# Kernel tuning notes

Measured on AMD Instinct MI355X. Metric: run time of the kernel, lower is better.

## Reference

```python
import math
import jax, jax.numpy as jnp
import numpy as np

N_HEADS = 16
N_KV_HEADS = 4
HEAD_DIM = 128
D_MODEL = 2048
THETA = 10000.0
SCALE_BASE = 512


def _rope_cos_sin(seq_len, head_dim, theta):
    half = head_dim // 2
    inv_freq = 1.0 / theta ** (jnp.arange(half, dtype=jnp.float32) / half)
    pos = jnp.arange(seq_len, dtype=jnp.float32)
    freqs = jnp.outer(pos, inv_freq)  # (S, half)
    freqs = jnp.concatenate([freqs, freqs], axis=-1)  # (S, D)
    return jnp.cos(freqs), jnp.sin(freqs)


def _rotate_half(x):
    half = x.shape[-1] // 2
    return jnp.concatenate([-x[..., half:], x[..., :half]], axis=-1)


def _xpos_scale(seq_len, head_dim, scale_base):
    pos = jnp.arange(seq_len, dtype=jnp.float32)
    scale = (pos + scale_base / 2.0) / scale_base  # (S,)
    half = head_dim // 2
    s = jnp.broadcast_to(scale[:, None], (seq_len, half))
    # interleave: even idx -> scale, odd idx -> 1/scale
    return jnp.stack([s, 1.0 / s], axis=-1).reshape(seq_len, head_dim)


def setup_inputs() -> dict:
    key = jax.random.key(0)
    ks = jax.random.split(key, 5)
    std = 1.0 / math.sqrt(D_MODEL)
    x = jax.random.normal(ks[0], (2, 2048, D_MODEL), dtype=jnp.float32)
    Wq = jax.random.normal(ks[1], (D_MODEL, N_HEADS * HEAD_DIM), dtype=jnp.float32) * std
    Wk = jax.random.normal(ks[2], (D_MODEL, N_KV_HEADS * HEAD_DIM), dtype=jnp.float32) * std
    Wv = jax.random.normal(ks[3], (D_MODEL, N_KV_HEADS * HEAD_DIM), dtype=jnp.float32) * std
    Wo = jax.random.normal(ks[4], (N_HEADS * HEAD_DIM, D_MODEL), dtype=jnp.float32) * std
    return {"x": x, "Wq": Wq, "Wk": Wk, "Wv": Wv, "Wo": Wo}


def reference(x, Wq, Wk, Wv, Wo):
    B, S, _ = x.shape
    kv_groups = N_HEADS // N_KV_HEADS

    q = (x @ Wq).reshape(B, S, N_HEADS, HEAD_DIM).transpose(0, 2, 1, 3)     # (B,H,S,D)
    k = (x @ Wk).reshape(B, S, N_KV_HEADS, HEAD_DIM).transpose(0, 2, 1, 3)  # (B,Hk,S,D)
    v = (x @ Wv).reshape(B, S, N_KV_HEADS, HEAD_DIM).transpose(0, 2, 1, 3)

    cos, sin = _rope_cos_sin(S, HEAD_DIM, THETA)
    cos = cos[None, None]
    sin = sin[None, None]
    q = q * cos + _rotate_half(q) * sin
    k = k * cos + _rotate_half(k) * sin
    xscale = _xpos_scale(S, HEAD_DIM, SCALE_BASE)[None, None]
    q = q * xscale
    k = k * (1.0 / xscale)

    # GQA: expand kv heads to full head count
    k = jnp.repeat(k, kv_groups, axis=1)  # (B,H,S,D)
    v = jnp.repeat(v, kv_groups, axis=1)

    scale = math.sqrt(HEAD_DIM)
    scores = jnp.einsum('bhqd,bhkd->bhqk', q, k) / scale
    causal = jnp.tril(jnp.ones((S, S), dtype=bool))
    scores = jnp.where(causal[None, None], scores, -jnp.inf)
    attn = jax.nn.softmax(scores, axis=-1)
    out = jnp.einsum('bhqk,bhkd->bhqd', attn, v)
    out = out.transpose(0, 2, 1, 3).reshape(B, S, N_HEADS * HEAD_DIM)
    return out @ Wo
```

## Files before the change

### kernel.cpp

```cpp
#include <hip/hip_runtime.h>
#include <math.h>

#define BDIM 2
#define SLEN 2048
#define NH 16
#define NKV 4
#define HD 128

typedef __attribute__((ext_vector_type(8))) short short8v;
typedef __attribute__((ext_vector_type(4))) short short4v;
typedef __attribute__((ext_vector_type(8))) __bf16 bf16x8;
typedef __attribute__((ext_vector_type(4))) float f32x4;
typedef __attribute__((ext_vector_type(16))) float f32x16;
typedef __attribute__((ext_vector_type(4))) unsigned int u32x4;

__device__ inline unsigned short f2bf(float x) {
  unsigned int u = __builtin_bit_cast(unsigned int, x);
  unsigned int r = (u + 0x7fffu + ((u >> 16) & 1u)) >> 16;
  return (unsigned short)r;
}
__device__ inline float bf2f(unsigned short b) {
  unsigned int u = ((unsigned int)b) << 16;
  return __builtin_bit_cast(float, u);
}
__device__ inline unsigned int pk2(float a, float b) {
  unsigned short ua = __builtin_bit_cast(unsigned short, (__bf16)a);
  unsigned short ub = __builtin_bit_cast(unsigned short, (__bf16)b);
  return (unsigned int)ua | ((unsigned int)ub << 16);
}

template <bool BF16_OUT, bool SPLIT>
__global__ __launch_bounds__(256) void gemm_mfma_bt(
    const unsigned short* __restrict__ A, const unsigned short* __restrict__ Bt,
    void* __restrict__ C0, void* __restrict__ C1,
    int M, int N, int K, int Nsplit, int S0, int S1) {
  __shared__ __align__(16) unsigned short As[128 * 64];
  __shared__ __align__(16) unsigned short Bs[128 * 64];
  const int t    = threadIdx.x;
  const int lane = t & 63;
  const int w    = t >> 6;
  const int lg   = lane >> 4, l15 = lane & 15;
  const int wr   = w >> 1,    wc  = w & 1;
  const int bm = blockIdx.y * 128, bn = blockIdx.x * 128;

  const int srow = w * 32 + (lane >> 3);
  const int scol = (lane & 7) * 8;
  const unsigned short* gA = &A[(size_t)(bm + srow) * K + scol];
  const unsigned short* gB = &Bt[(size_t)(bn + srow) * K + scol];

  f32x4 acc[4][4];
#pragma unroll
  for (int m = 0; m < 4; ++m)
#pragma unroll
    for (int n = 0; n < 4; ++n) acc[m][n] = (f32x4){0.f, 0.f, 0.f, 0.f};

  for (int k0 = 0; k0 < K; k0 += 64) {
    __syncthreads();
#pragma unroll
    for (int i = 0; i < 4; ++i) {
      __builtin_amdgcn_global_load_lds(
          (const __attribute__((address_space(1))) unsigned int*)(gA + (size_t)i * 8 * K + k0),
          (__attribute__((address_space(3))) unsigned int*)&As[(w * 32 + i * 8) * 64],
          16, 0, 0);
      __builtin_amdgcn_global_load_lds(
          (const __attribute__((address_space(1))) unsigned int*)(gB + (size_t)i * 8 * K + k0),
          (__attribute__((address_space(3))) unsigned int*)&Bs[(w * 32 + i * 8) * 64],
          16, 0, 0);
    }
    __syncthreads();
#pragma unroll
    for (int kk = 0; kk < 2; ++kk) {
      bf16x8 a[4], b[4];
#pragma unroll
      for (int m = 0; m < 4; ++m)
        a[m] = __builtin_bit_cast(bf16x8, *reinterpret_cast<const short8v*>(
            &As[(wr * 64 + m * 16 + l15) * 64 + kk * 32 + lg * 8]));
#pragma unroll
      for (int n = 0; n < 4; ++n)
        b[n] = __builtin_bit_cast(bf16x8, *reinterpret_cast<const short8v*>(
            &Bs[(wc * 64 + n * 16 + l15) * 64 + kk * 32 + lg * 8]));
#pragma unroll
      for (int m = 0; m < 4; ++m)
#pragma unroll
        for (int n = 0; n < 4; ++n)
          acc[m][n] = __builtin_amdgcn_mfma_f32_16x16x32_bf16(a[m], b[n], acc[m][n], 0, 0, 0);
    }
  }

  void* dst;
  int col0, stride;
  if (!SPLIT || bn < Nsplit) {
    dst = C0; col0 = bn; stride = S0;
  } else {
    dst = C1; col0 = bn - Nsplit; stride = S1;
  }
#pragma unroll
  for (int m = 0; m < 4; ++m) {
#pragma unroll
    for (int j = 0; j < 4; ++j) {
      const size_t row = (size_t)(bm + wr * 64 + m * 16 + lg * 4 + j);
#pragma unroll
      for (int n = 0; n < 4; ++n) {
        const int col = col0 + wc * 64 + n * 16 + l15;
        if (BF16_OUT)
          ((unsigned short*)dst)[row * stride + col] = f2bf(acc[m][n][j]);
        else
          ((float*)dst)[row * stride + col] = acc[m][n][j];
      }
    }
  }
}

__global__ __launch_bounds__(256) void transpose_cast(
    const float* __restrict__ W, unsigned short* __restrict__ Wt, int K, int N) {
  __shared__ float tile[32][33];
  const int tx = threadIdx.x & 31, ty = threadIdx.x >> 5;
  const int n0 = blockIdx.x * 32, k0 = blockIdx.y * 32;
#pragma unroll
  for (int i = 0; i < 4; ++i)
    tile[ty + i * 8][tx] = W[(size_t)(k0 + ty + i * 8) * N + n0 + tx];
  __syncthreads();
#pragma unroll
  for (int i = 0; i < 4; ++i)
    Wt[(size_t)(n0 + ty + i * 8) * K + k0 + tx] = f2bf(tile[tx][ty + i * 8]);
}

__global__ __launch_bounds__(256) void cast_f32_bf16(
    const float* __restrict__ in, unsigned short* __restrict__ out) {
  const int i = (blockIdx.x * 256 + threadIdx.x) * 8;
  float4 a = *reinterpret_cast<const float4*>(&in[i]);
  float4 b = *reinterpret_cast<const float4*>(&in[i + 4]);
  short8v s;
  s[0] = f2bf(a.x); s[1] = f2bf(a.y); s[2] = f2bf(a.z); s[3] = f2bf(a.w);
  s[4] = f2bf(b.x); s[5] = f2bf(b.y); s[6] = f2bf(b.z); s[7] = f2bf(b.w);
  *reinterpret_cast<short8v*>(&out[i]) = s;
}

__global__ __launch_bounds__(256) void rope_xpos_ip(
    unsigned short* __restrict__ buf, int row_stride, int nh_shift, int invert,
    float extra_scale) {
  const int idx = blockIdx.x * 256 + threadIdx.x;
  const int dp  = idx & 63;
  const int tmp = idx >> 6;
  const int h   = tmp & ((1 << nh_shift) - 1);
  const int row = tmp >> nh_shift;
  const int s   = row & (SLEN - 1);

  const float inv_freq = expf(-(float)dp * (9.210340371976184f / 64.0f));
  const float ang = (float)s * inv_freq;
  float sn, cs;
  sincosf(ang, &sn, &cs);

  unsigned short* p = buf + (size_t)row * row_stride + h * HD;
  const float x0 = bf2f(p[dp]);
  const float x1 = bf2f(p[dp + 64]);
  float y0 = x0 * cs - x1 * sn;
  float y1 = x1 * cs + x0 * sn;

  const float scl = ((float)s + 256.0f) / 512.0f;
  float se_even = invert ? (1.0f / scl) : scl;
  float se_odd  = invert ? scl : (1.0f / scl);
  float se = ((dp & 1) ? se_odd : se_even) * extra_scale;

  p[dp]      = f2bf(y0 * se);
  p[dp + 64] = f2bf(y1 * se);
}

__global__ __launch_bounds__(512) void flash_attn_v9(
    const unsigned short* __restrict__ qb, const unsigned short* __restrict__ kvb,
    unsigned short* __restrict__ o) {
  const int bid = blockIdx.x;
  const int u   = bid & 7;
  const int bh  = bid >> 3;
  const int h   = bh & (NH - 1);
  const int b   = bh >> 4;
  const int kvh = h >> 2;

  __shared__ __align__(16) unsigned char smem[65536];

  const int t    = threadIdx.x;
  const int lane = t & 63;
  const int w    = t >> 6;
  const int par  = w >> 2;
  const int wq   = w & 3;
  const int hi   = lane >> 5;
  const int l31  = lane & 31;

  const size_t bS = (size_t)b * SLEN;

  const int vr2 = t & 31;
  const int vg  = t >> 5;
  int krow[2], kgrp[2];
#pragma unroll
  for (int i = 0; i < 2; ++i) {
    const int slot = w * 2048 + i * 1024 + lane * 16;
    krow[i] = slot >> 8;
    kgrp[i] = (slot >> 4) & 15;
  }

#define K_STAGE(kt, bufk)                                                      \
  { _Pragma("unroll") for (int i = 0; i < 2; ++i) {                            \
      const unsigned short* ksrc = &kvb[(bS + (size_t)(kt) * 64 + krow[i]) * 1024 \
          + kvh * 128 + ((kgrp[i] ^ (krow[i] & 15)) << 3)];                    \
      __builtin_amdgcn_global_load_lds(                                        \
          (const __attribute__((address_space(1))) unsigned int*)ksrc,         \
          (__attribute__((address_space(3))) unsigned int*)                    \
              (smem + (bufk) * 16384 + w * 2048 + i * 1024),                   \
          16, 0, 0); } }

#define V_LOAD(kt, r0, r1)                                                     \
  { const size_t vb_ = (bS + (size_t)(kt) * 64) * 1024 + kvh * 128 + 512;      \
    r0 = *reinterpret_cast<const short8v*>(                                    \
        &kvb[vb_ + (size_t)(2 * vr2) * 1024 + vg * 8]);                        \
    r1 = *reinterpret_cast<const short8v*>(                                    \
        &kvb[vb_ + (size_t)(2 * vr2 + 1) * 1024 + vg * 8]); }

#define V_WRITE(bufk, r0, r1)                                                  \
  { unsigned int* Vw_ = (unsigned int*)(smem + 32768 + (bufk) * 16384);        \
    _Pragma("unroll") for (int j = 0; j < 8; ++j) {                            \
      const int d = vg * 8 + j;                                                \
      Vw_[d * 32 + (vr2 ^ ((d & 7) << 2))] =                                   \
          (unsigned int)(unsigned short)r0[j] |                                \
          ((unsigned int)(unsigned short)r1[j] << 16); } }

  for (int half = 0; half < 2; ++half) {
    const int qt2 = half ? (15 - u) : u;

    bf16x8 qf[8];
    {
      const size_t qrow = (bS + qt2 * 128 + wq * 32 + l31) * 2048 + (size_t)h * HD;
#pragma unroll
      for (int c = 0; c < 8; ++c)
        qf[c] = __builtin_bit_cast(bf16x8,
            *reinterpret_cast<const short8v*>(&qb[qrow + c * 16 + hi * 8]));
    }

    f32x16 Od[4];
#pragma unroll
    for (int ds = 0; ds < 4; ++ds)
#pragma unroll
      for (int r = 0; r < 16; ++r) Od[ds][r] = 0.f;
    float m_run = -1e30f, l_run = 0.f;

    short8v va0, va1, vb0, vb1;

    K_STAGE(0, 0)
    K_STAGE(1, 1)
    V_LOAD(0, va0, va1)
    V_LOAD(1, vb0, vb1)
    V_WRITE(0, va0, va1)
    V_WRITE(1, vb0, vb1)
    __syncthreads();

    for (int e = 0; e <= qt2; ++e) {
      const int kt = 2 * e + par;
      const bool more = (e < qt2);
      if (more) {
        V_LOAD(2 * e + 2, va0, va1)
        V_LOAD(2 * e + 3, vb0, vb1)
      }
      const unsigned short* Kb = (const unsigned short*)(smem + par * 16384);
      const unsigned int*   Vw = (const unsigned int*)(smem + 32768 + par * 16384);

      f32x16 Sa, Sb;
#pragma unroll
      for (int r = 0; r < 16; ++r) { Sa[r] = 0.f; Sb[r] = 0.f; }
      __builtin_amdgcn_s_setprio(1);
#pragma unroll
      for (int c = 0; c < 8; ++c) {
        const int ra = l31, rb = 32 + l31;
        bf16x8 ka = __builtin_bit_cast(bf16x8, *reinterpret_cast<const short8v*>(
            &Kb[ra * 128 + (((2 * c + hi) ^ (ra & 15)) << 3)]));
        bf16x8 kb2 = __builtin_bit_cast(bf16x8, *reinterpret_cast<const short8v*>(
            &Kb[rb * 128 + (((2 * c + hi) ^ (rb & 15)) << 3)]));
        Sa = __builtin_amdgcn_mfma_f32_32x32x16_bf16(ka, qf[c], Sa, 0, 0, 0);
        Sb = __builtin_amdgcn_mfma_f32_32x32x16_bf16(kb2, qf[c], Sb, 0, 0, 0);
      }
      __builtin_amdgcn_s_setprio(0);

      if (kt >= 2 * qt2) {
        const int thresh = qt2 * 128 + wq * 32 + l31 - kt * 64;
#pragma unroll
        for (int r = 0; r < 16; ++r) {
          const int kla = (r & 3) + 8 * (r >> 2) + 4 * hi;
          if (kla > thresh) Sa[r] = -INFINITY;
          if (kla + 32 > thresh) Sb[r] = -INFINITY;
        }
      }

      float pmax = Sa[0];
#pragma unroll
      for (int r = 0; r < 16; ++r) pmax = fmaxf(pmax, fmaxf(Sa[r], Sb[r]));
      pmax = fmaxf(pmax, __shfl_xor(pmax, 32));

      const bool defer = __all(pmax - m_run <= 8.0f);
      float m_new, f;
      if (defer) {
        m_new = m_run; f = 1.0f;
      } else {
        m_new = fmaxf(m_run, pmax);
        f = __expf(m_run - m_new);
        m_run = m_new;
      }

      float psum = 0.f;
#pragma unroll
      for (int r = 0; r < 16; ++r) {
        Sa[r] = __expf(Sa[r] - m_new);
        Sb[r] = __expf(Sb[r] - m_new);
        psum += Sa[r] + Sb[r];
      }
      psum += __shfl_xor(psum, 32);
      l_run = l_run * f + psum;

      if (!defer) {
#pragma unroll
        for (int ds = 0; ds < 4; ++ds)
#pragma unroll
          for (int r = 0; r < 16; ++r) Od[ds][r] *= f;
      }

#pragma unroll
      for (int kc = 0; kc < 4; ++kc) {
        const int Zz = kc & 1;
        f32x16 Sx = (kc >> 1) ? Sb : Sa;
        unsigned int W00 = pk2(Sx[4 * (2 * Zz + 0) + 0], Sx[4 * (2 * Zz + 0) + 1]);
        unsigned int W01 = pk2(Sx[4 * (2 * Zz + 0) + 2], Sx[4 * (2 * Zz + 0) + 3]);
        unsigned int W10 = pk2(Sx[4 * (2 * Zz + 1) + 0], Sx[4 * (2 * Zz + 1) + 1]);
        unsigned int W11 = pk2(Sx[4 * (2 * Zz + 1) + 2], Sx[4 * (2 * Zz + 1) + 3]);
        unsigned int X00 = __shfl_xor(W00, 32), X01 = __shfl_xor(W01, 32);
        unsigned int X10 = __shfl_xor(W10, 32), X11 = __shfl_xor(W11, 32);
        u32x4 pv;
        pv[0] = hi ? X10 : W00;
        pv[1] = hi ? X11 : W01;
        pv[2] = hi ? W10 : X00;
        pv[3] = hi ? W11 : X01;
        bf16x8 pf = __builtin_bit_cast(bf16x8, pv);
        __builtin_amdgcn_s_setprio(1);
#pragma unroll
        for (int ds = 0; ds < 4; ++ds) {
          const int d = ds * 32 + l31;
          u32x4 vv = *reinterpret_cast<const u32x4*>(
              &Vw[d * 32 + ((kc * 8 + hi * 4) ^ ((d & 7) << 2))]);
          bf16x8 vf = __builtin_bit_cast(bf16x8, vv);
          Od[ds] = __builtin_amdgcn_mfma_f32_32x32x16_bf16(vf, pf, Od[ds], 0, 0, 0);
        }
        __builtin_amdgcn_s_setprio(0);
      }

      __syncthreads();
      if (more) {
        K_STAGE(2 * e + 2, 0)
        K_STAGE(2 * e + 3, 1)
        V_WRITE(0, va0, va1)
        V_WRITE(1, vb0, vb1)
        __syncthreads();
      }
    }

    __syncthreads();
    float* mf = (float*)smem;
    float* Of = (float*)(smem + 2048);
    if (par == 1) {
      mf[(wq * 2 + 0) * 64 + lane] = m_run;
      mf[(wq * 2 + 1) * 64 + lane] = l_run;
    }
    float fe = 0.f, fo = 0.f, linv = 0.f;
#pragma unroll
    for (int p = 0; p < 2; ++p) {
      if (par == 1) {
#pragma unroll
        for (int d2 = 0; d2 < 2; ++d2)
#pragma unroll
          for (int r = 0; r < 16; ++r)
            Of[((wq * 2 + d2) * 16 + r) * 64 + lane] = Od[p * 2 + d2][r];
      }
      __syncthreads();
      if (par == 0) {
        if (p == 0) {
          const float m_o = mf[(wq * 2 + 0) * 64 + lane];
          const float l_o = mf[(wq * 2 + 1) * 64 + lane];
          const float mm = fmaxf(m_run, m_o);
          fe = __expf(m_run - mm);
          fo = __expf(m_o - mm);
          linv = 1.0f / (l_run * fe + l_o * fo);
        }
        const size_t row = bS + qt2 * 128 + wq * 32 + l31;
#pragma unroll
        for (int d2 = 0; d2 < 2; ++d2) {
          const int ds = p * 2 + d2;
#pragma unroll
          for (int g = 0; g < 4; ++g) {
            short4v ov;
#pragma unroll
            for (int j = 0; j < 4; ++j) {
              const int r = g * 4 + j;
              const float val = (Od[ds][r] * fe +
                                 Of[((wq * 2 + d2) * 16 + r) * 64 + lane] * fo) * linv;
              ov[j] = (short)__builtin_bit_cast(unsigned short, (__bf16)val);
            }
            const int dbase = ds * 32 + 8 * g + 4 * hi;
            *reinterpret_cast<short4v*>(&o[row * 2048 + h * HD + dbase]) = ov;
          }
        }
      }
      __syncthreads();
    }
  }
#undef K_STAGE
#undef V_LOAD
#undef V_WRITE
}

extern "C" void kernel_launch(void* const* d_in, const int* in_sizes, int n_in,
                              void* d_out, int out_size, void* d_ws, size_t ws_size,
                              hipStream_t stream) {
  (void)in_sizes; (void)n_in; (void)out_size; (void)ws_size;
  const float* x  = (const float*)d_in[0];
  const float* Wq = (const float*)d_in[1];
  const float* Wk = (const float*)d_in[2];
  const float* Wv = (const float*)d_in[3];
  const float* Wo = (const float*)d_in[4];
  float* out = (float*)d_out;

  unsigned char* ws = (unsigned char*)d_ws;
  const size_t MB = 1024 * 1024;
  unsigned short* xb    = (unsigned short*)(ws);
  unsigned short* Wqkvt = (unsigned short*)(ws + 16 * MB);
  unsigned short* Wot   = (unsigned short*)(ws + 28 * MB);
  unsigned short* qb    = (unsigned short*)(ws + 36 * MB);
  unsigned short* kvb   = (unsigned short*)(ws + 52 * MB);
  unsigned short* attn  = (unsigned short*)(ws + 60 * MB);

  const int M = BDIM * SLEN;
  dim3 blk(256);

  cast_f32_bf16<<<(M * 2048) / (256 * 8), blk, 0, stream>>>(x, xb);
  transpose_cast<<<dim3(64, 64), blk, 0, stream>>>(Wq, Wqkvt, 2048, 2048);
  transpose_cast<<<dim3(16, 64), blk, 0, stream>>>(
      Wk, Wqkvt + (size_t)2048 * 2048, 2048, 512);
  transpose_cast<<<dim3(16, 64), blk, 0, stream>>>(
      Wv, Wqkvt + (size_t)2560 * 2048, 2048, 512);
  transpose_cast<<<dim3(64, 64), blk, 0, stream>>>(Wo, Wot, 2048, 2048);

  gemm_mfma_bt<true, true><<<dim3(24, 32), blk, 0, stream>>>(
      xb, Wqkvt, qb, kvb, M, 3072, 2048, 2048, 2048, 1024);

  rope_xpos_ip<<<(M * NH * 64) / 256, blk, 0, stream>>>(
      qb, 2048, 4, 0, 0.088388347648318447f);
  rope_xpos_ip<<<(M * NKV * 64) / 256, blk, 0, stream>>>(kvb, 1024, 2, 1, 1.0f);

  flash_attn_v9<<<BDIM * NH * 8, dim3(512), 0, stream>>>(qb, kvb, attn);

  gemm_mfma_bt<false, false><<<dim3(16, 32), blk, 0, stream>>>(
      attn, Wot, out, nullptr, M, 2048, 2048, 2048, 2048, 0);
}
```

Measured before the change: 245.3 us.

## Pipeline GEMM K-loop with triple-buffered LDS ring and XOR-swizzled tiles

Replaces the single-buffered GEMM main loop, which synchronised twice per 64-wide K step, with a three-slot LDS ring over 32-wide K tiles. Tiles are prefetched two steps ahead via global_load_lds, and explicit vmcnt waits let loads overlap the MFMA work. It also XOR-swizzles the LDS column chunks to reduce bank conflicts on fragment reads. The cost is more LDS per block (48KB), which may lower occupancy, and twice as many barrier rounds because the K step is smaller.

```diff
diff --git a/kernel.cpp b/kernel.cpp
--- a/kernel.cpp
+++ b/kernel.cpp
@@ -30,12 +30,11 @@
 }
 
 template <bool BF16_OUT, bool SPLIT>
-__global__ __launch_bounds__(256) void gemm_mfma_bt(
+__global__ __launch_bounds__(256) void gemm_ring(
     const unsigned short* __restrict__ A, const unsigned short* __restrict__ Bt,
     void* __restrict__ C0, void* __restrict__ C1,
     int M, int N, int K, int Nsplit, int S0, int S1) {
-  __shared__ __align__(16) unsigned short As[128 * 64];
-  __shared__ __align__(16) unsigned short Bs[128 * 64];
+  __shared__ __align__(16) unsigned short lds[3 * 8192];
   const int t    = threadIdx.x;
   const int lane = t & 63;
   const int w    = t >> 6;
@@ -43,10 +42,25 @@
   const int wr   = w >> 1,    wc  = w & 1;
   const int bm = blockIdx.y * 128, bn = blockIdx.x * 128;
 
-  const int srow = w * 32 + (lane >> 3);
-  const int scol = (lane & 7) * 8;
-  const unsigned short* gA = &A[(size_t)(bm + srow) * K + scol];
-  const unsigned short* gB = &Bt[(size_t)(bn + srow) * K + scol];
+  const int r0  = t >> 2;
+  const int c8  = (t & 3) ^ (r0 & 3);
+  const int dst = t * 8;
+
+#define STAGE(kt, b)                                                           \
+  { _Pragma("unroll") for (int i = 0; i < 2; ++i) {                            \
+      __builtin_amdgcn_global_load_lds(                                        \
+          (const __attribute__((address_space(1))) unsigned int*)              \
+              &A[(size_t)(bm + i * 64 + r0) * K + (kt) * 32 + c8 * 8],         \
+          (__attribute__((address_space(3))) unsigned int*)                    \
+              &lds[(b) * 8192 + i * 2048 + dst],                               \
+          16, 0, 0);                                                           \
+      __builtin_amdgcn_global_load_lds(                                        \
+          (const __attribute__((address_space(1))) unsigned int*)              \
+              &Bt[(size_t)(bn + i * 64 + r0) * K + (kt) * 32 + c8 * 8],        \
+          (__attribute__((address_space(3))) unsigned int*)                    \
+              &lds[(b) * 8192 + 4096 + i * 2048 + dst],                        \
+          16, 0, 0);                                                           \
+  } }
 
   f32x4 acc[4][4];
 #pragma unroll
@@ -54,45 +68,57 @@
 #pragma unroll
     for (int n = 0; n < 4; ++n) acc[m][n] = (f32x4){0.f, 0.f, 0.f, 0.f};
 
-  for (int k0 = 0; k0 < K; k0 += 64) {
-    __syncthreads();
-#pragma unroll
-    for (int i = 0; i < 4; ++i) {
-      __builtin_amdgcn_global_load_lds(
-          (const __attribute__((address_space(1))) unsigned int*)(gA + (size_t)i * 8 * K + k0),
-          (__attribute__((address_space(3))) unsigned int*)&As[(w * 32 + i * 8) * 64],
-          16, 0, 0);
-      __builtin_amdgcn_global_load_lds(
-          (const __attribute__((address_space(1))) unsigned int*)(gB + (size_t)i * 8 * K + k0),
-          (__attribute__((address_space(3))) unsigned int*)&Bs[(w * 32 + i * 8) * 64],
-          16, 0, 0);
-    }
-    __syncthreads();
-#pragma unroll
-    for (int kk = 0; kk < 2; ++kk) {
-      bf16x8 a[4], b[4];
-#pragma unroll
-      for (int m = 0; m < 4; ++m)
-        a[m] = __builtin_bit_cast(bf16x8, *reinterpret_cast<const short8v*>(
-            &As[(wr * 64 + m * 16 + l15) * 64 + kk * 32 + lg * 8]));
+  const int NT = K >> 5;
+  STAGE(0, 0)
+  STAGE(1, 1)
+  int bc = 0;
+
+  for (int kt = 0; kt < NT; ++kt) {
+    if (kt + 1 < NT) {
+      asm volatile("s_waitcnt vmcnt(4)" ::: "memory");
+    } else {
+      asm volatile("s_waitcnt vmcnt(0)" ::: "memory");
+    }
+    __builtin_amdgcn_s_barrier();
+    __builtin_amdgcn_sched_barrier(0);
+
+    const unsigned short* As = &lds[bc * 8192];
+    const unsigned short* Bs = As + 4096;
+    bf16x8 a[4], b[4];
+#pragma unroll
+    for (int m = 0; m < 4; ++m) {
+      const int row = wr * 64 + m * 16 + l15;
+      a[m] = __builtin_bit_cast(bf16x8, *reinterpret_cast<const short8v*>(
+          &As[row * 32 + ((lg ^ (l15 & 3)) * 8)]));
+    }
+#pragma unroll
+    for (int n = 0; n < 4; ++n) {
+      const int row = wc * 64 + n * 16 + l15;
+      b[n] = __builtin_bit_cast(bf16x8, *reinterpret_cast<const short8v*>(
+          &Bs[row * 32 + ((lg ^ (l15 & 3)) * 8)]));
+    }
+#pragma unroll
+    for (int m = 0; m < 4; ++m)
 #pragma unroll
       for (int n = 0; n < 4; ++n)
-        b[n] = __builtin_bit_cast(bf16x8, *reinterpret_cast<const short8v*>(
-            &Bs[(wc * 64 + n * 16 + l15) * 64 + kk * 32 + lg * 8]));
-#pragma unroll
-      for (int m = 0; m < 4; ++m)
-#pragma unroll
-        for (int n = 0; n < 4; ++n)
-          acc[m][n] = __builtin_amdgcn_mfma_f32_16x16x32_bf16(a[m], b[n], acc[m][n], 0, 0, 0);
-    }
+        acc[m][n] = __builtin_amdgcn_mfma_f32_16x16x32_bf16(a[m], b[n], acc[m][n], 0, 0, 0);
+
+    asm volatile("s_waitcnt lgkmcnt(0)" ::: "memory");
+    __builtin_amdgcn_s_barrier();
+    __builtin_amdgcn_sched_barrier(0);
+    if (kt + 2 < NT) {
+      const int nb = bc + 2 >= 3 ? bc - 1 : bc + 2;
+      STAGE(kt + 2, nb)
+    }
+    bc = (bc + 1 >= 3) ? 0 : bc + 1;
   }
 
-  void* dst;
+  void* dst_p;
   int col0, stride;
   if (!SPLIT || bn < Nsplit) {
-    dst = C0; col0 = bn; stride = S0;
+    dst_p = C0; col0 = bn; stride = S0;
   } else {
-    dst = C1; col0 = bn - Nsplit; stride = S1;
+    dst_p = C1; col0 = bn - Nsplit; stride = S1;
   }
 #pragma unroll
   for (int m = 0; m < 4; ++m) {
@@ -103,12 +129,13 @@
       for (int n = 0; n < 4; ++n) {
         const int col = col0 + wc * 64 + n * 16 + l15;
         if (BF16_OUT)
-          ((unsigned short*)dst)[row * stride + col] = f2bf(acc[m][n][j]);
+          ((unsigned short*)dst_p)[row * stride + col] = f2bf(acc[m][n][j]);
         else
-          ((float*)dst)[row * stride + col] = acc[m][n][j];
+          ((float*)dst_p)[row * stride + col] = acc[m][n][j];
       }
     }
   }
+#undef STAGE
 }
 
 __global__ __launch_bounds__(256) void transpose_cast(
@@ -443,7 +470,7 @@
       Wv, Wqkvt + (size_t)2560 * 2048, 2048, 512);
   transpose_cast<<<dim3(64, 64), blk, 0, stream>>>(Wo, Wot, 2048, 2048);
 
-  gemm_mfma_bt<true, true><<<dim3(24, 32), blk, 0, stream>>>(
+  gemm_ring<true, true><<<dim3(24, 32), blk, 0, stream>>>(
       xb, Wqkvt, qb, kvb, M, 3072, 2048, 2048, 2048, 1024);
 
   rope_xpos_ip<<<(M * NH * 64) / 256, blk, 0, stream>>>(
@@ -452,6 +479,6 @@
 
   flash_attn_v9<<<BDIM * NH * 8, dim3(512), 0, stream>>>(qb, kvb, attn);
 
-  gemm_mfma_bt<false, false><<<dim3(16, 32), blk, 0, stream>>>(
+  gemm_ring<false, false><<<dim3(16, 32), blk, 0, stream>>>(
       attn, Wot, out, nullptr, M, 2048, 2048, 2048, 2048, 0);
 }
```

After: 220.1 us. 10.3% less time.
